# Optimization experiments

Hardware: AMD Instinct MI355X
Metric: run time of the kernel (lower is better)

Reference implementation:

```python
import jax, jax.numpy as jnp
import numpy as np

EMBED_DIM = 1024
NUM_HEADS = 16
HEAD_DIM = EMBED_DIM // NUM_HEADS


def setup_inputs() -> dict:
    key = jax.random.key(0)
    ks = jax.random.split(key, 9)
    B, S, D = 4, 2048, EMBED_DIM
    scale = 1.0 / np.sqrt(D)
    inp = {
        "x": jax.random.normal(ks[0], (B, S, D), dtype=jnp.float32),
        "wq": jax.random.normal(ks[1], (D, D), dtype=jnp.float32) * scale,
        "bq": jnp.zeros((D,), dtype=jnp.float32),
        "wk": jax.random.normal(ks[2], (D, D), dtype=jnp.float32) * scale,
        "bk": jnp.zeros((D,), dtype=jnp.float32),
        "wv": jax.random.normal(ks[3], (D, D), dtype=jnp.float32) * scale,
        "bv": jnp.zeros((D,), dtype=jnp.float32),
        "wo": jax.random.normal(ks[4], (D, D), dtype=jnp.float32) * scale,
        "bo": jnp.zeros((D,), dtype=jnp.float32),
    }
    return inp


def reference(x, wq, bq, wk, bk, wv, bv, wo, bo):
    B, S, D = x.shape
    H, Hd = NUM_HEADS, HEAD_DIM

    def split_heads(t):
        # [B, S, D] -> [B, H, S, Hd]
        return t.reshape(B, S, H, Hd).transpose(0, 2, 1, 3)

    q = split_heads(x @ wq.T + bq)
    k = split_heads(x @ wk.T + bk)
    v = split_heads(x @ wv.T + bv)

    scores = jnp.einsum("bhqd,bhkd->bhqk", q, k) / jnp.sqrt(jnp.float32(Hd))
    attn = jax.nn.softmax(scores, axis=-1)
    out = jnp.einsum("bhqk,bhkd->bhqd", attn, v)  # [B, H, S, Hd]
    out = out.transpose(0, 2, 1, 3).reshape(B, S, D)
    return out @ wo.T + bo
```

## Files before the change

kernel.cpp:

```cpp
#include <hip/hip_runtime.h>
#include <hip/hip_bf16.h>
#include <hip/hip_fp16.h>

typedef _Float16 f16;
typedef f16 f16x8 __attribute__((ext_vector_type(8)));
typedef f16 f16x4 __attribute__((ext_vector_type(4)));
typedef f16 f16x2 __attribute__((ext_vector_type(2)));
typedef float f32x4 __attribute__((ext_vector_type(4)));
typedef float f32x16 __attribute__((ext_vector_type(16)));
typedef unsigned int u32x4 __attribute__((ext_vector_type(4)));
typedef unsigned int u32x2 __attribute__((ext_vector_type(2)));

#define MFMA16(a, b, c) __builtin_amdgcn_mfma_f32_16x16x32_f16(a, b, c, 0, 0, 0)
#define MFMA32(a, b, c) __builtin_amdgcn_mfma_f32_32x32x16_f16(a, b, c, 0, 0, 0)

constexpr int BB = 4, SS = 2048, DD = 1024, HH = 16, HDIM = 64;
constexpr int MM = BB * SS;
constexpr float QSCALE = 0.125f * 1.44269504088896340736f;


__device__ __forceinline__ void gl_lds16(const void* g, void* l) {
  __builtin_amdgcn_global_load_lds((const __attribute__((address_space(1))) void*)g,
                                   (__attribute__((address_space(3))) void*)l, 16, 0, 0);
}

__global__ __launch_bounds__(256) void cvt_all_kernel(const float* __restrict__ x,
                                                      const float* __restrict__ w0,
                                                      const float* __restrict__ w1,
                                                      const float* __restrict__ w2,
                                                      const float* __restrict__ w3,
                                                      f16* xh, f16* o0, f16* o1,
                                                      f16* o2, f16* o3) {
  int bid = blockIdx.x;
  const float* in; f16* out; int idx;
  if (bid < MM * DD / 4 / 256) {
    in = x; out = xh; idx = bid * 256 + threadIdx.x;
  } else {
    int wb = bid - MM * DD / 4 / 256;
    int which = wb >> 10;
    in = which == 0 ? w0 : which == 1 ? w1 : which == 2 ? w2 : w3;
    out = which == 0 ? o0 : which == 1 ? o1 : which == 2 ? o2 : o3;
    idx = (wb & 1023) * 256 + threadIdx.x;
  }
  f32x4 v = reinterpret_cast<const f32x4*>(in)[idx];
  f16x4 o;
  o[0] = (f16)v[0]; o[1] = (f16)v[1]; o[2] = (f16)v[2]; o[3] = (f16)v[3];
  reinterpret_cast<f16x4*>(out)[idx] = o;
}

__device__ __forceinline__ int swz(int row, int slot) {
  return row * 64 + ((slot ^ (row & 7)) << 3);
}

__global__ __launch_bounds__(256) void qkv_kernel(const f16* __restrict__ A,
                                                  const f16* __restrict__ Wq,
                                                  const f16* __restrict__ Wk,
                                                  const f16* __restrict__ Wv,
                                                  const float* __restrict__ bq,
                                                  const float* __restrict__ bk,
                                                  const float* __restrict__ bv,
                                                  f16* __restrict__ Qo,
                                                  f16* __restrict__ Ko,
                                                  f16* __restrict__ Vo) {
  constexpr int K = 1024;
  constexpr int TS = 152;
  __shared__ __align__(16) char smem_raw[128 * TS * 2];
  f16* As = (f16*)smem_raw;
  f16* Ws = As + 128 * 64;

  const int p = blockIdx.x;
  const int bx = (p >> 3) % 24;
  const int by = (p & 7) + 8 * ((p >> 3) / 24);

  const int mat = bx >> 3;
  const f16* W = mat == 0 ? Wq : (mat == 1 ? Wk : Wv);
  const float* bias = mat == 0 ? bq : (mat == 1 ? bk : bv);
  const float scale = mat == 0 ? QSCALE : 1.0f;

  const int tid = threadIdx.x;
  const int m0 = by * 128, n0 = (bx & 7) * 128;
  const int w = tid >> 6, lane = tid & 63;
  const int wm = (w >> 1) * 64, wn = (w & 1) * 64;
  const int g = lane >> 4, r = lane & 15;
  const int srow = lane >> 3;
  const int sslot = (lane & 7) ^ srow;

  f32x4 acc[4][4] = {};

  for (int k0 = 0; k0 < K; k0 += 64) {
#pragma unroll
    for (int i = 0; i < 4; ++i) {
      int rbase = w * 32 + i * 8;
      gl_lds16(A + (size_t)(m0 + rbase + srow) * K + k0 + sslot * 8, As + rbase * 64);
      gl_lds16(W + (size_t)(n0 + rbase + srow) * K + k0 + sslot * 8, Ws + rbase * 64);
    }
    __syncthreads();

#pragma unroll
    for (int ks = 0; ks < 2; ++ks) {
      f16x8 af[4], bf[4];
#pragma unroll
      for (int i = 0; i < 4; ++i) {
        af[i] = *reinterpret_cast<const f16x8*>(As + swz(wm + i * 16 + r, (ks << 2) | g));
        bf[i] = *reinterpret_cast<const f16x8*>(Ws + swz(wn + i * 16 + r, (ks << 2) | g));
      }
#pragma unroll
      for (int i = 0; i < 4; ++i)
#pragma unroll
        for (int j = 0; j < 4; ++j)
          acc[i][j] = MFMA16(af[i], bf[j], acc[i][j]);
    }
    __syncthreads();
  }

  if (mat == 0) {
#pragma unroll
    for (int i = 0; i < 4; ++i)
#pragma unroll
      for (int j = 0; j < 4; ++j)
#pragma unroll
        for (int q = 0; q < 4; ++q) {
          int gm = m0 + wm + i * 16 + g * 4 + q;
          int gn = n0 + wn + j * 16 + r;
          float v = (acc[i][j][q] + bias[gn]) * scale;
          int b = gm >> 11, s = gm & 2047;
          int h = gn >> 6, hd = gn & 63;
          Qo[(((size_t)(b * HH + h)) * SS + s) * HDIM + hd] = (f16)v;
        }
  } else if (mat == 1) {
    __syncthreads();
    f16* T = (f16*)smem_raw;
#pragma unroll
    for (int i = 0; i < 4; ++i)
#pragma unroll
      for (int j = 0; j < 4; ++j)
#pragma unroll
        for (int q = 0; q < 4; ++q) {
          int ml = wm + i * 16 + g * 4 + q;
          int nl = wn + j * 16 + r;
          T[ml * TS + nl] = (f16)(acc[i][j][q] + bias[n0 + nl]);
        }
    __syncthreads();
    const int b = m0 >> 11, sbase = m0 & 2047;
#pragma unroll
    for (int it = 0; it < 8; ++it) {
      int cid = it * 256 + tid;
      int row_s = cid & 127, ns = cid >> 7;
      u32x4 v = *reinterpret_cast<const u32x4*>(T + row_s * TS + ns * 8);
      int gn0 = n0 + ns * 8;
      int h = gn0 >> 6, slot = (gn0 & 63) >> 3;
      int tile = (sbase >> 6) + (row_s >> 6), row = row_s & 63;
      size_t off = ((((size_t)(b * HH + h) * 32 + tile) * 8 + slot) * 64 + row) * 8;
      *reinterpret_cast<u32x4*>(Ko + off) = v;
    }
  } else {
    __syncthreads();
    f16* T = (f16*)smem_raw;
#pragma unroll
    for (int i = 0; i < 4; ++i)
#pragma unroll
      for (int j = 0; j < 4; ++j)
#pragma unroll
        for (int q = 0; q < 4; ++q) {
          int ml = wm + i * 16 + g * 4 + q;
          int nl = wn + j * 16 + r;
          T[nl * TS + ml] = (f16)(acc[i][j][q] + bias[n0 + nl]);
        }
    __syncthreads();
    const int b = m0 >> 11, sbase = m0 & 2047;
#pragma unroll
    for (int it = 0; it < 8; ++it) {
      int cid = it * 256 + tid;
      int hd_l = cid & 127, sl = (cid >> 7) & 7, tl = cid >> 10;
      u32x4 v = *reinterpret_cast<const u32x4*>(T + hd_l * TS + tl * 64 + sl * 8);
      int gn = n0 + hd_l, h = gn >> 6, hd = gn & 63;
      int tile = (sbase >> 6) + tl;
      size_t off = ((((size_t)(b * HH + h) * 32 + tile) * 8 + sl) * 64 + hd) * 8;
      *reinterpret_cast<u32x4*>(Vo + off) = v;
    }
  }
}

__global__ __launch_bounds__(256) void oproj_kernel(const f16* __restrict__ A,
                                                    const f16* __restrict__ W,
                                                    const float* __restrict__ bias,
                                                    float* __restrict__ Out) {
  constexpr int K = 1024, N = 1024;
  __shared__ __align__(16) f16 As[128 * 64];
  __shared__ __align__(16) f16 Ws[128 * 64];

  const int p = blockIdx.x;
  const int bx = (p >> 3) & 7;
  const int by = (p & 7) | ((p >> 6) << 3);

  const int tid = threadIdx.x;
  const int m0 = by * 128, n0 = bx * 128;
  const int w = tid >> 6, lane = tid & 63;
  const int wm = (w >> 1) * 64, wn = (w & 1) * 64;
  const int g = lane >> 4, r = lane & 15;
  const int srow = lane >> 3;
  const int sslot = (lane & 7) ^ srow;

  f32x4 acc[4][4] = {};

  for (int k0 = 0; k0 < K; k0 += 64) {
#pragma unroll
    for (int i = 0; i < 4; ++i) {
      int rbase = w * 32 + i * 8;
      gl_lds16(A + (size_t)(m0 + rbase + srow) * K + k0 + sslot * 8, As + rbase * 64);
      gl_lds16(W + (size_t)(n0 + rbase + srow) * K + k0 + sslot * 8, Ws + rbase * 64);
    }
    __syncthreads();

#pragma unroll
    for (int ks = 0; ks < 2; ++ks) {
      f16x8 af[4], bf[4];
#pragma unroll
      for (int i = 0; i < 4; ++i) {
        af[i] = *reinterpret_cast<const f16x8*>(As + swz(wm + i * 16 + r, (ks << 2) | g));
        bf[i] = *reinterpret_cast<const f16x8*>(Ws + swz(wn + i * 16 + r, (ks << 2) | g));
      }
#pragma unroll
      for (int i = 0; i < 4; ++i)
#pragma unroll
        for (int j = 0; j < 4; ++j)
          acc[i][j] = MFMA16(af[i], bf[j], acc[i][j]);
    }
    __syncthreads();
  }

#pragma unroll
  for (int i = 0; i < 4; ++i)
#pragma unroll
    for (int j = 0; j < 4; ++j)
#pragma unroll
      for (int q = 0; q < 4; ++q) {
        int gm = m0 + wm + i * 16 + g * 4 + q;
        int gn = n0 + wn + j * 16 + r;
        Out[(size_t)gm * N + gn] = acc[i][j][q] + bias[gn];
      }
}

__global__ __launch_bounds__(256, 2) void attn_kernel(const f16* __restrict__ Q,
                                                      const f16* __restrict__ K,
                                                      const f16* __restrict__ Vt,
                                                      f16* __restrict__ AO) {
  __shared__ __align__(16) f16 Kls[2][8 * 512];
  __shared__ __align__(16) f16 Vls[3][8 * 512];
  __shared__ __align__(16) float Lw[4][64];

  const int p = blockIdx.x;
  const int qx = (p >> 3) & 7;
  const int bh = (p & 7) | ((p >> 6) << 3);
  const int q0 = qx * 256;

  const int tid = threadIdx.x;
  const int w = tid >> 6, lane = tid & 63;
  const int q31 = lane & 31;
  const int h = lane >> 5;
  const f16* Kg = K + (size_t)bh * (SS * HDIM);
  const f16* Vg = Vt + (size_t)bh * (SS * HDIM);
  const int s0 = 2 * w;
  const int rofs = h * 512 + q31 * 8;

  const f16* Qg = Q + ((size_t)bh * SS + q0 + w * 64 + q31) * HDIM + 8 * h;
  f16x8 qf[2][4];
#pragma unroll
  for (int f = 0; f < 2; ++f)
#pragma unroll
    for (int m = 0; m < 4; ++m)
      qf[f][m] = *reinterpret_cast<const f16x8*>(Qg + f * 32 * HDIM + 16 * m);

  f32x16 oacc[2][2] = {};
  float lsum0 = 0.f, lsum1 = 0.f;
  unsigned pkP0[8], pkP1[8];

#pragma unroll
  for (int i = 0; i < 2; ++i) {
    int s_idx = s0 + i;
    gl_lds16(Kg + (size_t)(s_idx * 64 + lane) * 8, &Kls[0][s_idx * 512]);
    gl_lds16(Vg + (size_t)(s_idx * 64 + lane) * 8, &Vls[0][s_idx * 512]);
  }
  __syncthreads();

#define QK_PHASE(KC, KB, SC0, SC1)                                                   \
  do {                                                                               \
    _Pragma("unroll") for (int m = 0; m < 4; ++m) {                                  \
      f16x8 kf = *reinterpret_cast<const f16x8*>((KC) + m * 1024 + (KB)*256 + rofs); \
      SC0 = MFMA32(kf, qf[0][m], SC0);                                               \
      SC1 = MFMA32(kf, qf[1][m], SC1);                                               \
    }                                                                                \
  } while (0)

#define PV_PHASE(VPTR, JB)                                                               \
  do {                                                                                   \
    _Pragma("unroll") for (int jl = 0; jl < 2; ++jl) {                                   \
      auto a0 = __builtin_amdgcn_permlane32_swap(pkP0[4 * jl + 0], pkP0[4 * jl + 2],     \
                                                 false, false);                          \
      auto a1 = __builtin_amdgcn_permlane32_swap(pkP0[4 * jl + 1], pkP0[4 * jl + 3],     \
                                                 false, false);                          \
      u32x4 fa = {(unsigned)a0[0], (unsigned)a1[0], (unsigned)a0[1], (unsigned)a1[1]};   \
      f16x8 pa0 = __builtin_bit_cast(f16x8, fa);                                         \
      auto b0 = __builtin_amdgcn_permlane32_swap(pkP1[4 * jl + 0], pkP1[4 * jl + 2],     \
                                                 false, false);                          \
      auto b1 = __builtin_amdgcn_permlane32_swap(pkP1[4 * jl + 1], pkP1[4 * jl + 3],     \
                                                 false, false);                          \
      u32x4 fb = {(unsigned)b0[0], (unsigned)b1[0], (unsigned)b0[1], (unsigned)b1[1]};   \
      f16x8 pa1 = __builtin_bit_cast(f16x8, fb);                                         \
      const int j = (JB) + jl;                                                           \
      _Pragma("unroll") for (int vb = 0; vb < 2; ++vb) {                                 \
        f16x8 vbf = *reinterpret_cast<const f16x8*>((VPTR) + j * 1024 + vb * 256 + rofs);\
        oacc[0][vb] = MFMA32(pa0, vbf, oacc[0][vb]);                                     \
        oacc[1][vb] = MFMA32(pa1, vbf, oacc[1][vb]);                                     \
      }                                                                                  \
    }                                                                                    \
  } while (0)

#define SM_PHASE(SC0, SC1)                                                               \
  do {                                                                                   \
    _Pragma("unroll") for (int rp = 0; rp < 4; ++rp)                                     \
        _Pragma("unroll") for (int pp = 0; pp < 2; ++pp) {                               \
      float a0 = __builtin_amdgcn_exp2f((SC0)[4 * rp + 2 * pp]);                         \
      float a1 = __builtin_amdgcn_exp2f((SC0)[4 * rp + 2 * pp + 1]);                     \
      pkP0[2 * rp + pp] = __builtin_bit_cast(unsigned, __builtin_amdgcn_cvt_pkrtz(a0, a1));\
      float b0 = __builtin_amdgcn_exp2f((SC1)[4 * rp + 2 * pp]);                         \
      float b1 = __builtin_amdgcn_exp2f((SC1)[4 * rp + 2 * pp + 1]);                     \
      pkP1[2 * rp + pp] = __builtin_bit_cast(unsigned, __builtin_amdgcn_cvt_pkrtz(b0, b1));\
    }                                                                                    \
    {                                                                                    \
      f16x2 u01 = __builtin_bit_cast(f16x2, pkP0[0]) + __builtin_bit_cast(f16x2, pkP0[1]);\
      f16x2 u23 = __builtin_bit_cast(f16x2, pkP0[2]) + __builtin_bit_cast(f16x2, pkP0[3]);\
      f16x2 u45 = __builtin_bit_cast(f16x2, pkP0[4]) + __builtin_bit_cast(f16x2, pkP0[5]);\
      f16x2 u67 = __builtin_bit_cast(f16x2, pkP0[6]) + __builtin_bit_cast(f16x2, pkP0[7]);\
      f16x2 ut = (u01 + u23) + (u45 + u67);                                              \
      lsum0 += (float)ut[0] + (float)ut[1];                                              \
    }                                                                                    \
    {                                                                                    \
      f16x2 u01 = __builtin_bit_cast(f16x2, pkP1[0]) + __builtin_bit_cast(f16x2, pkP1[1]);\
      f16x2 u23 = __builtin_bit_cast(f16x2, pkP1[2]) + __builtin_bit_cast(f16x2, pkP1[3]);\
      f16x2 u45 = __builtin_bit_cast(f16x2, pkP1[4]) + __builtin_bit_cast(f16x2, pkP1[5]);\
      f16x2 u67 = __builtin_bit_cast(f16x2, pkP1[6]) + __builtin_bit_cast(f16x2, pkP1[7]);\
      f16x2 ut = (u01 + u23) + (u45 + u67);                                              \
      lsum1 += (float)ut[0] + (float)ut[1];                                              \
    }                                                                                    \
  } while (0)

  for (int t = 0; t < SS / 64; ++t) {
    if (t < SS / 64 - 1) {
      f16* kdst = &Kls[(t + 1) & 1][0];
      f16* vdst = &Vls[(t + 1) % 3][0];
#pragma unroll
      for (int i = 0; i < 2; ++i) {
        int s_idx = s0 + i;
        gl_lds16(Kg + (size_t)((t + 1) * 512 + s_idx * 64 + lane) * 8, kdst + s_idx * 512);
        gl_lds16(Vg + (size_t)((t + 1) * 512 + s_idx * 64 + lane) * 8, vdst + s_idx * 512);
      }
    }
    const f16* Kc = &Kls[t & 1][0];
    const f16* Vcur = &Vls[t % 3][0];
    const f16* Vprev = &Vls[(t + 2) % 3][0];

    {
      f32x16 sc0 = {}, sc1 = {};
      __builtin_amdgcn_s_setprio(1);
      QK_PHASE(Kc, 0, sc0, sc1);
      if (t > 0) PV_PHASE(Vprev, 2);
      __builtin_amdgcn_s_setprio(0);
      SM_PHASE(sc0, sc1);
    }
    {
      f32x16 sc0 = {}, sc1 = {};
      __builtin_amdgcn_s_setprio(1);
      QK_PHASE(Kc, 1, sc0, sc1);
      PV_PHASE(Vcur, 0);
      __builtin_amdgcn_s_setprio(0);
      SM_PHASE(sc0, sc1);
    }
    __syncthreads();
  }

  {
    const f16* Vlast = &Vls[(SS / 64 - 1) % 3][0];
    __builtin_amdgcn_s_setprio(1);
    PV_PHASE(Vlast, 2);
    __builtin_amdgcn_s_setprio(0);
  }

  lsum0 += __shfl_xor(lsum0, 32, 64);
  lsum1 += __shfl_xor(lsum1, 32, 64);
  if (h == 0) {
    Lw[w][q31] = 1.0f / lsum0;
    Lw[w][32 + q31] = 1.0f / lsum1;
  }

  const int b = bh >> 4, head = bh & 15;
#pragma unroll
  for (int f = 0; f < 2; ++f) {
    f32x4 li[4];
#pragma unroll
    for (int rq = 0; rq < 4; ++rq)
      li[rq] = *reinterpret_cast<const f32x4*>(&Lw[w][32 * f + 8 * rq + 4 * h]);
    f16* aobase = AO + ((size_t)(b * SS + q0 + 64 * w + 32 * f)) * DD + head * 64 + q31;
#pragma unroll
    for (int vb = 0; vb < 2; ++vb)
#pragma unroll
      for (int reg = 0; reg < 16; ++reg) {
        int q = (reg & 3) + 8 * (reg >> 2) + 4 * h;
        aobase[(size_t)q * DD + 32 * vb] = (f16)(oacc[f][vb][reg] * li[reg >> 2][reg & 3]);
      }
  }
#undef QK_PHASE
#undef PV_PHASE
#undef SM_PHASE
}

extern "C" void kernel_launch(void* const* d_in, const int* in_sizes, int n_in,
                              void* d_out, int out_size, void* d_ws, size_t ws_size,
                              hipStream_t stream) {
  (void)in_sizes; (void)n_in; (void)out_size; (void)ws_size;
  const float* x  = (const float*)d_in[0];
  const float* wq = (const float*)d_in[1];
  const float* bq = (const float*)d_in[2];
  const float* wk = (const float*)d_in[3];
  const float* bk = (const float*)d_in[4];
  const float* wv = (const float*)d_in[5];
  const float* bv = (const float*)d_in[6];
  const float* wo = (const float*)d_in[7];
  const float* bo = (const float*)d_in[8];
  float* out = (float*)d_out;

  char* ws = (char*)d_ws;
  f16* xh  = (f16*)ws; ws += (size_t)MM * DD * 2;
  f16* wqh = (f16*)ws; ws += (size_t)DD * DD * 2;
  f16* wkh = (f16*)ws; ws += (size_t)DD * DD * 2;
  f16* wvh = (f16*)ws; ws += (size_t)DD * DD * 2;
  f16* woh = (f16*)ws; ws += (size_t)DD * DD * 2;
  f16* Qb  = (f16*)ws; ws += (size_t)MM * DD * 2;
  f16* Kb  = (f16*)ws; ws += (size_t)MM * DD * 2;
  f16* Vtb = (f16*)ws; ws += (size_t)MM * DD * 2;
  f16* AOb = (f16*)ws; ws += (size_t)MM * DD * 2;

  cvt_all_kernel<<<MM * DD / 4 / 256 + 4 * (DD * DD / 4 / 256), 256, 0, stream>>>(
      x, wq, wk, wv, wo, xh, wqh, wkh, wvh, woh);

  qkv_kernel<<<1536, 256, 0, stream>>>(xh, wqh, wkh, wvh, bq, bk, bv, Qb, Kb, Vtb);

  attn_kernel<<<512, 256, 0, stream>>>(Qb, Kb, Vtb, AOb);

  oproj_kernel<<<512, 256, 0, stream>>>(AOb, woh, bo, out);
}
```

Before: 179.7 us.

## Load K/V tiles directly from global memory into registers instead of LDS staging

The attention kernel drops the LDS double/triple buffers for K and V along with the per-iteration __syncthreads. Each wave now loads its own K and V fragments straight from global memory into registers and prefetches the next tile during the softmax phase. This removes the LDS round trip and the block-wide barriers. In exchange, each of the four waves in a block reloads the same K/V data from global memory (relying on cache), and register pressure rises, which may hurt occupancy.

```diff
diff --git a/kernel.cpp b/kernel.cpp
--- a/kernel.cpp
+++ b/kernel.cpp
@@ -245,9 +245,7 @@
                                                       const f16* __restrict__ K,
                                                       const f16* __restrict__ Vt,
                                                       f16* __restrict__ AO) {
-  __shared__ __align__(16) f16 Kls[2][8 * 512];
-  __shared__ __align__(16) f16 Vls[3][8 * 512];
-  __shared__ __align__(16) float Lw[4][64];
+  __shared__ float Lw[4][64];
 
   const int p = blockIdx.x;
   const int qx = (p >> 3) & 7;
@@ -258,10 +256,9 @@
   const int w = tid >> 6, lane = tid & 63;
   const int q31 = lane & 31;
   const int h = lane >> 5;
-  const f16* Kg = K + (size_t)bh * (SS * HDIM);
-  const f16* Vg = Vt + (size_t)bh * (SS * HDIM);
-  const int s0 = 2 * w;
-  const int rofs = h * 512 + q31 * 8;
+
+  const f16* Kl = K + (size_t)bh * (SS * HDIM) + h * 512 + q31 * 8;
+  const f16* Vl = Vt + (size_t)bh * (SS * HDIM) + h * 512 + q31 * 8;
 
   const f16* Qg = Q + ((size_t)bh * SS + q0 + w * 64 + q31) * HDIM + 8 * h;
   f16x8 qf[2][4];
@@ -275,24 +272,21 @@
   float lsum0 = 0.f, lsum1 = 0.f;
   unsigned pkP0[8], pkP1[8];
 
-#pragma unroll
-  for (int i = 0; i < 2; ++i) {
-    int s_idx = s0 + i;
-    gl_lds16(Kg + (size_t)(s_idx * 64 + lane) * 8, &Kls[0][s_idx * 512]);
-    gl_lds16(Vg + (size_t)(s_idx * 64 + lane) * 8, &Vls[0][s_idx * 512]);
-  }
-  __syncthreads();
-
-#define QK_PHASE(KC, KB, SC0, SC1)                                                   \
-  do {                                                                               \
-    _Pragma("unroll") for (int m = 0; m < 4; ++m) {                                  \
-      f16x8 kf = *reinterpret_cast<const f16x8*>((KC) + m * 1024 + (KB)*256 + rofs); \
-      SC0 = MFMA32(kf, qf[0][m], SC0);                                               \
-      SC1 = MFMA32(kf, qf[1][m], SC1);                                               \
-    }                                                                                \
-  } while (0)
-
-#define PV_PHASE(VPTR, JB)                                                               \
+  u32x4 kA[4], kB[4], vLo[4], vHi[4];
+
+#define LD16(PTR) (*reinterpret_cast<const u32x4*>(PTR))
+
+#pragma unroll
+  for (int m = 0; m < 4; ++m) kA[m] = LD16(Kl + m * 1024);
+#pragma unroll
+  for (int m = 0; m < 4; ++m) kB[m] = LD16(Kl + m * 1024 + 256);
+#pragma unroll
+  for (int jl = 0; jl < 2; ++jl)
+#pragma unroll
+    for (int vb = 0; vb < 2; ++vb)
+      vLo[2 * jl + vb] = LD16(Vl + jl * 1024 + vb * 256);
+
+#define PV_CLUSTER(VREG)                                                                 \
   do {                                                                                   \
     _Pragma("unroll") for (int jl = 0; jl < 2; ++jl) {                                   \
       auto a0 = __builtin_amdgcn_permlane32_swap(pkP0[4 * jl + 0], pkP0[4 * jl + 2],     \
@@ -307,16 +301,15 @@
                                                  false, false);                          \
       u32x4 fb = {(unsigned)b0[0], (unsigned)b1[0], (unsigned)b0[1], (unsigned)b1[1]};   \
       f16x8 pa1 = __builtin_bit_cast(f16x8, fb);                                         \
-      const int j = (JB) + jl;                                                           \
       _Pragma("unroll") for (int vb = 0; vb < 2; ++vb) {                                 \
-        f16x8 vbf = *reinterpret_cast<const f16x8*>((VPTR) + j * 1024 + vb * 256 + rofs);\
+        f16x8 vbf = __builtin_bit_cast(f16x8, (VREG)[2 * jl + vb]);                      \
         oacc[0][vb] = MFMA32(pa0, vbf, oacc[0][vb]);                                     \
         oacc[1][vb] = MFMA32(pa1, vbf, oacc[1][vb]);                                     \
       }                                                                                  \
     }                                                                                    \
   } while (0)
 
-#define SM_PHASE(SC0, SC1)                                                               \
+#define SM_CLUSTER(SC0, SC1)                                                             \
   do {                                                                                   \
     _Pragma("unroll") for (int rp = 0; rp < 4; ++rp)                                     \
         _Pragma("unroll") for (int pp = 0; pp < 2; ++pp) {                               \
@@ -346,45 +339,59 @@
   } while (0)
 
   for (int t = 0; t < SS / 64; ++t) {
-    if (t < SS / 64 - 1) {
-      f16* kdst = &Kls[(t + 1) & 1][0];
-      f16* vdst = &Vls[(t + 1) % 3][0];
-#pragma unroll
-      for (int i = 0; i < 2; ++i) {
-        int s_idx = s0 + i;
-        gl_lds16(Kg + (size_t)((t + 1) * 512 + s_idx * 64 + lane) * 8, kdst + s_idx * 512);
-        gl_lds16(Vg + (size_t)((t + 1) * 512 + s_idx * 64 + lane) * 8, vdst + s_idx * 512);
-      }
-    }
-    const f16* Kc = &Kls[t & 1][0];
-    const f16* Vcur = &Vls[t % 3][0];
-    const f16* Vprev = &Vls[(t + 2) % 3][0];
+    const size_t tb = (size_t)t * 4096;
+    const size_t tn = tb + 4096;
 
     {
       f32x16 sc0 = {}, sc1 = {};
       __builtin_amdgcn_s_setprio(1);
-      QK_PHASE(Kc, 0, sc0, sc1);
-      if (t > 0) PV_PHASE(Vprev, 2);
+#pragma unroll
+      for (int m = 0; m < 4; ++m) {
+        f16x8 kf = __builtin_bit_cast(f16x8, kA[m]);
+        sc0 = MFMA32(kf, qf[0][m], sc0);
+        sc1 = MFMA32(kf, qf[1][m], sc1);
+      }
+      if (t > 0) PV_CLUSTER(vHi);
       __builtin_amdgcn_s_setprio(0);
-      SM_PHASE(sc0, sc1);
-    }
+#pragma unroll
+      for (int jl = 0; jl < 2; ++jl)
+#pragma unroll
+        for (int vb = 0; vb < 2; ++vb)
+          vHi[2 * jl + vb] = LD16(Vl + tb + (2 + jl) * 1024 + vb * 256);
+      if (t < SS / 64 - 1) {
+#pragma unroll
+        for (int m = 0; m < 4; ++m) kA[m] = LD16(Kl + tn + m * 1024);
+      }
+      SM_CLUSTER(sc0, sc1);
+    }
+
     {
       f32x16 sc0 = {}, sc1 = {};
       __builtin_amdgcn_s_setprio(1);
-      QK_PHASE(Kc, 1, sc0, sc1);
-      PV_PHASE(Vcur, 0);
+#pragma unroll
+      for (int m = 0; m < 4; ++m) {
+        f16x8 kf = __builtin_bit_cast(f16x8, kB[m]);
+        sc0 = MFMA32(kf, qf[0][m], sc0);
+        sc1 = MFMA32(kf, qf[1][m], sc1);
+      }
+      PV_CLUSTER(vLo);
       __builtin_amdgcn_s_setprio(0);
-      SM_PHASE(sc0, sc1);
-    }
-    __syncthreads();
-  }
-
-  {
-    const f16* Vlast = &Vls[(SS / 64 - 1) % 3][0];
-    __builtin_amdgcn_s_setprio(1);
-    PV_PHASE(Vlast, 2);
-    __builtin_amdgcn_s_setprio(0);
-  }
+      if (t < SS / 64 - 1) {
+#pragma unroll
+        for (int m = 0; m < 4; ++m) kB[m] = LD16(Kl + tn + m * 1024 + 256);
+#pragma unroll
+        for (int jl = 0; jl < 2; ++jl)
+#pragma unroll
+          for (int vb = 0; vb < 2; ++vb)
+            vLo[2 * jl + vb] = LD16(Vl + tn + jl * 1024 + vb * 256);
+      }
+      SM_CLUSTER(sc0, sc1);
+    }
+  }
+
+  __builtin_amdgcn_s_setprio(1);
+  PV_CLUSTER(vHi);
+  __builtin_amdgcn_s_setprio(0);
 
   lsum0 += __shfl_xor(lsum0, 32, 64);
   lsum1 += __shfl_xor(lsum1, 32, 64);
@@ -409,9 +416,9 @@
         aobase[(size_t)q * DD + 32 * vb] = (f16)(oacc[f][vb][reg] * li[reg >> 2][reg & 3]);
       }
   }
-#undef QK_PHASE
-#undef PV_PHASE
-#undef SM_PHASE
+#undef PV_CLUSTER
+#undef SM_CLUSTER
+#undef LD16
 }
 
 extern "C" void kernel_launch(void* const* d_in, const int* in_sizes, int n_in,
```

Result: slower. 184.6 us (+2.7%).

## Replace QKV and output GEMMs with triple-buffered 256x128 eight-wave kernel

Applied to the files above, without the earlier changes.

Merges the QKV and output-projection GEMMs into one templated kernel with 256x128 tiles, 512 threads, and a three-stage LDS ring. Prefetches for tile t+2 are issued between MFMA phases, with vmcnt-based waits and raised wave priority so loads overlap compute. The goal is to hide global-to-LDS latency and raise MFMA density over the single-buffered, sync-heavy originals. In exchange it uses much more LDS per block (about 144 KB), which limits occupancy, and launches fewer blocks (768 and 256), which may underfill the GPU's CUs.

```diff
diff --git a/kernel.cpp b/kernel.cpp
--- a/kernel.cpp
+++ b/kernel.cpp
@@ -48,197 +48,218 @@
   reinterpret_cast<f16x4*>(out)[idx] = o;
 }
 
-__device__ __forceinline__ int swz(int row, int slot) {
-  return row * 64 + ((slot ^ (row & 7)) << 3);
-}
-
-__global__ __launch_bounds__(256) void qkv_kernel(const f16* __restrict__ A,
-                                                  const f16* __restrict__ Wq,
-                                                  const f16* __restrict__ Wk,
-                                                  const f16* __restrict__ Wv,
-                                                  const float* __restrict__ bq,
-                                                  const float* __restrict__ bk,
-                                                  const float* __restrict__ bv,
-                                                  f16* __restrict__ Qo,
-                                                  f16* __restrict__ Ko,
-                                                  f16* __restrict__ Vo) {
-  constexpr int K = 1024;
-  constexpr int TS = 152;
-  __shared__ __align__(16) char smem_raw[128 * TS * 2];
-  f16* As = (f16*)smem_raw;
-  f16* Ws = As + 128 * 64;
+template <bool QKV>
+__global__ __launch_bounds__(512) void gemm8_kernel(const f16* __restrict__ A,
+                                                    const f16* __restrict__ W0,
+                                                    const f16* __restrict__ W1,
+                                                    const f16* __restrict__ W2,
+                                                    const float* __restrict__ b0,
+                                                    const float* __restrict__ b1,
+                                                    const float* __restrict__ b2,
+                                                    void* __restrict__ O0,
+                                                    void* __restrict__ O1,
+                                                    void* __restrict__ O2) {
+  constexpr int NT = 16;
+  constexpr int BUF = 256 * 64 + 128 * 64;
+  __shared__ __align__(16) f16 smem[3 * BUF];
 
   const int p = blockIdx.x;
-  const int bx = (p >> 3) % 24;
-  const int by = (p & 7) + 8 * ((p >> 3) / 24);
-
-  const int mat = bx >> 3;
-  const f16* W = mat == 0 ? Wq : (mat == 1 ? Wk : Wv);
-  const float* bias = mat == 0 ? bq : (mat == 1 ? bk : bv);
-  const float scale = mat == 0 ? QSCALE : 1.0f;
+  const int bl = p >> 3;
+  const int NS = QKV ? 24 : 8;
+  const int nn = bl % NS;
+  const int my = (p & 7) + 8 * (bl / NS);
+  const int mat = QKV ? (nn >> 3) : 0;
+  const int m0 = my * 256;
+  const int n0 = (nn & 7) * 128;
+
+  const f16* W = mat == 0 ? W0 : (mat == 1 ? W1 : W2);
+  const float* bias = mat == 0 ? b0 : (mat == 1 ? b1 : b2);
 
   const int tid = threadIdx.x;
-  const int m0 = by * 128, n0 = (bx & 7) * 128;
   const int w = tid >> 6, lane = tid & 63;
-  const int wm = (w >> 1) * 64, wn = (w & 1) * 64;
+  const int wm = w >> 2, wn = w & 3;
   const int g = lane >> 4, r = lane & 15;
-  const int srow = lane >> 3;
-  const int sslot = (lane & 7) ^ srow;
-
-  f32x4 acc[4][4] = {};
-
-  for (int k0 = 0; k0 < K; k0 += 64) {
-#pragma unroll
-    for (int i = 0; i < 4; ++i) {
-      int rbase = w * 32 + i * 8;
-      gl_lds16(A + (size_t)(m0 + rbase + srow) * K + k0 + sslot * 8, As + rbase * 64);
-      gl_lds16(W + (size_t)(n0 + rbase + srow) * K + k0 + sslot * 8, Ws + rbase * 64);
-    }
+
+  const int srow_a = ((w * 64 + lane) >> 3);
+  const int sc = lane & 7;
+
+  f32x4 acc[8][2] = {};
+
+#define STAGE_A(I, PB, KT)                                                              \
+  do {                                                                                  \
+    int cid_ = ((I)*8 + w) * 64 + lane;                                                 \
+    int row_ = cid_ >> 3, c_ = cid_ & 7;                                                \
+    gl_lds16(A + (size_t)(m0 + row_) * 1024 + (KT) + ((c_ ^ (row_ & 7)) << 3),          \
+             smem + (PB) + ((I)*8 + w) * 512);                                          \
+  } while (0)
+#define STAGE_B(I, PB, KT)                                                              \
+  do {                                                                                  \
+    int cid_ = ((I)*8 + w) * 64 + lane;                                                 \
+    int row_ = cid_ >> 3, c_ = cid_ & 7;                                                \
+    gl_lds16(W + (size_t)(n0 + row_) * 1024 + (KT) + ((c_ ^ (row_ & 7)) << 3),          \
+             smem + (PB) + 256 * 64 + ((I)*8 + w) * 512);                               \
+  } while (0)
+
+#pragma unroll
+  for (int i = 0; i < 4; ++i) STAGE_A(i, 0, 0);
+#pragma unroll
+  for (int i = 0; i < 2; ++i) STAGE_B(i, 0, 0);
+#pragma unroll
+  for (int i = 0; i < 4; ++i) STAGE_A(i, BUF, 64);
+#pragma unroll
+  for (int i = 0; i < 2; ++i) STAGE_B(i, BUF, 64);
+  __builtin_amdgcn_sched_barrier(0);
+  asm volatile("s_waitcnt vmcnt(6)" ::: "memory");
+  __builtin_amdgcn_s_barrier();
+  __builtin_amdgcn_sched_barrier(0);
+
+  for (int t = 0; t < NT; ++t) {
+    const f16* Ab = smem + (t % 3) * BUF;
+    const f16* Wb = Ab + 256 * 64;
+    const int pb = ((t + 2) % 3) * BUF;
+    const int kpf = (t + 2) * 64;
+    const bool do_pf = (t + 2) < NT;
+
+    f16x8 wf[2][2];
+#pragma unroll
+    for (int ks = 0; ks < 2; ++ks)
+#pragma unroll
+      for (int j = 0; j < 2; ++j) {
+        int rowW = wn * 32 + j * 16 + r;
+        wf[ks][j] = *reinterpret_cast<const f16x8*>(
+            Wb + rowW * 64 + (((ks << 2) | g) ^ (rowW & 7)) * 8);
+      }
+
+    if (do_pf) { STAGE_A(0, pb, kpf); STAGE_A(1, pb, kpf); STAGE_B(0, pb, kpf); }
+    __builtin_amdgcn_s_setprio(1);
+#pragma unroll
+    for (int ks = 0; ks < 2; ++ks)
+#pragma unroll
+      for (int i = 0; i < 4; ++i) {
+        int rowA = wm * 128 + i * 16 + r;
+        f16x8 af = *reinterpret_cast<const f16x8*>(
+            Ab + rowA * 64 + (((ks << 2) | g) ^ (rowA & 7)) * 8);
+        acc[i][0] = MFMA16(af, wf[ks][0], acc[i][0]);
+        acc[i][1] = MFMA16(af, wf[ks][1], acc[i][1]);
+      }
+    __builtin_amdgcn_s_setprio(0);
+
+    if (do_pf) { STAGE_A(2, pb, kpf); STAGE_A(3, pb, kpf); STAGE_B(1, pb, kpf); }
+    __builtin_amdgcn_s_setprio(1);
+#pragma unroll
+    for (int ks = 0; ks < 2; ++ks)
+#pragma unroll
+      for (int i = 0; i < 4; ++i) {
+        int rowA = wm * 128 + 64 + i * 16 + r;
+        f16x8 af = *reinterpret_cast<const f16x8*>(
+            Ab + rowA * 64 + (((ks << 2) | g) ^ (rowA & 7)) * 8);
+        acc[4 + i][0] = MFMA16(af, wf[ks][0], acc[4 + i][0]);
+        acc[4 + i][1] = MFMA16(af, wf[ks][1], acc[4 + i][1]);
+      }
+    __builtin_amdgcn_s_setprio(0);
+
+    __builtin_amdgcn_sched_barrier(0);
+    if (t < NT - 2) {
+      asm volatile("s_waitcnt vmcnt(6)" ::: "memory");
+      __builtin_amdgcn_s_barrier();
+    } else if (t == NT - 2) {
+      asm volatile("s_waitcnt vmcnt(0)" ::: "memory");
+      __builtin_amdgcn_s_barrier();
+    }
+    __builtin_amdgcn_sched_barrier(0);
+  }
+#undef STAGE_A
+#undef STAGE_B
+
+  const int sbase = m0 & 2047, bb = m0 >> 11;
+  if constexpr (!QKV) {
+    float* Out = reinterpret_cast<float*>(O0);
+#pragma unroll
+    for (int ii = 0; ii < 8; ++ii) {
+      int rowoff = (ii >> 2) * 64 + (ii & 3) * 16;
+#pragma unroll
+      for (int j = 0; j < 2; ++j)
+#pragma unroll
+        for (int q = 0; q < 4; ++q) {
+          int gm = m0 + wm * 128 + rowoff + g * 4 + q;
+          int gn = n0 + wn * 32 + j * 16 + r;
+          Out[(size_t)gm * 1024 + gn] = acc[ii][j][q] + bias[gn];
+        }
+    }
+  } else if (mat == 0) {
+    f16* Qo = reinterpret_cast<f16*>(O0);
+#pragma unroll
+    for (int ii = 0; ii < 8; ++ii) {
+      int rowoff = (ii >> 2) * 64 + (ii & 3) * 16;
+#pragma unroll
+      for (int j = 0; j < 2; ++j)
+#pragma unroll
+        for (int q = 0; q < 4; ++q) {
+          int gm = m0 + wm * 128 + rowoff + g * 4 + q;
+          int gn = n0 + wn * 32 + j * 16 + r;
+          float v = (acc[ii][j][q] + bias[gn]) * QSCALE;
+          int b = gm >> 11, s = gm & 2047;
+          int hh = gn >> 6, hd = gn & 63;
+          Qo[(((size_t)(b * HH + hh)) * SS + s) * HDIM + hd] = (f16)v;
+        }
+    }
+  } else if (mat == 1) {
+    f16* Ko = reinterpret_cast<f16*>(O1);
     __syncthreads();
-
-#pragma unroll
-    for (int ks = 0; ks < 2; ++ks) {
-      f16x8 af[4], bf[4];
-#pragma unroll
-      for (int i = 0; i < 4; ++i) {
-        af[i] = *reinterpret_cast<const f16x8*>(As + swz(wm + i * 16 + r, (ks << 2) | g));
-        bf[i] = *reinterpret_cast<const f16x8*>(Ws + swz(wn + i * 16 + r, (ks << 2) | g));
-      }
-#pragma unroll
-      for (int i = 0; i < 4; ++i)
-#pragma unroll
-        for (int j = 0; j < 4; ++j)
-          acc[i][j] = MFMA16(af[i], bf[j], acc[i][j]);
+    f16* T = smem;
+#pragma unroll
+    for (int ii = 0; ii < 8; ++ii) {
+      int rowoff = (ii >> 2) * 64 + (ii & 3) * 16;
+#pragma unroll
+      for (int j = 0; j < 2; ++j)
+#pragma unroll
+        for (int q = 0; q < 4; ++q) {
+          int ml = wm * 128 + rowoff + g * 4 + q;
+          int nl = wn * 32 + j * 16 + r;
+          T[ml * 136 + nl] = (f16)(acc[ii][j][q] + bias[n0 + nl]);
+        }
     }
     __syncthreads();
-  }
-
-  if (mat == 0) {
-#pragma unroll
-    for (int i = 0; i < 4; ++i)
-#pragma unroll
-      for (int j = 0; j < 4; ++j)
+#pragma unroll
+    for (int it = 0; it < 8; ++it) {
+      int cid = it * 512 + tid;
+      int row_s = cid & 255, ns = cid >> 8;
+      u32x4 v = *reinterpret_cast<const u32x4*>(T + row_s * 136 + ns * 8);
+      int gn0 = n0 + ns * 8;
+      int hh = gn0 >> 6, slot = (gn0 & 63) >> 3;
+      int tile = (sbase >> 6) + (row_s >> 6), row = row_s & 63;
+      size_t off = ((((size_t)(bb * HH + hh) * 32 + tile) * 8 + slot) * 64 + row) * 8;
+      *reinterpret_cast<u32x4*>(Ko + off) = v;
+    }
+  } else {
+    f16* Vo = reinterpret_cast<f16*>(O2);
+    __syncthreads();
+    f16* T = smem;
+#pragma unroll
+    for (int ii = 0; ii < 8; ++ii) {
+      int rowoff = (ii >> 2) * 64 + (ii & 3) * 16;
+#pragma unroll
+      for (int j = 0; j < 2; ++j)
 #pragma unroll
         for (int q = 0; q < 4; ++q) {
-          int gm = m0 + wm + i * 16 + g * 4 + q;
-          int gn = n0 + wn + j * 16 + r;
-          float v = (acc[i][j][q] + bias[gn]) * scale;
-          int b = gm >> 11, s = gm & 2047;
-          int h = gn >> 6, hd = gn & 63;
-          Qo[(((size_t)(b * HH + h)) * SS + s) * HDIM + hd] = (f16)v;
+          int ml = wm * 128 + rowoff + g * 4 + q;
+          int nl = wn * 32 + j * 16 + r;
+          T[nl * 264 + ml] = (f16)(acc[ii][j][q] + bias[n0 + nl]);
         }
-  } else if (mat == 1) {
+    }
     __syncthreads();
-    f16* T = (f16*)smem_raw;
-#pragma unroll
-    for (int i = 0; i < 4; ++i)
-#pragma unroll
-      for (int j = 0; j < 4; ++j)
-#pragma unroll
-        for (int q = 0; q < 4; ++q) {
-          int ml = wm + i * 16 + g * 4 + q;
-          int nl = wn + j * 16 + r;
-          T[ml * TS + nl] = (f16)(acc[i][j][q] + bias[n0 + nl]);
-        }
-    __syncthreads();
-    const int b = m0 >> 11, sbase = m0 & 2047;
 #pragma unroll
     for (int it = 0; it < 8; ++it) {
-      int cid = it * 256 + tid;
-      int row_s = cid & 127, ns = cid >> 7;
-      u32x4 v = *reinterpret_cast<const u32x4*>(T + row_s * TS + ns * 8);
-      int gn0 = n0 + ns * 8;
-      int h = gn0 >> 6, slot = (gn0 & 63) >> 3;
-      int tile = (sbase >> 6) + (row_s >> 6), row = row_s & 63;
-      size_t off = ((((size_t)(b * HH + h) * 32 + tile) * 8 + slot) * 64 + row) * 8;
-      *reinterpret_cast<u32x4*>(Ko + off) = v;
-    }
-  } else {
-    __syncthreads();
-    f16* T = (f16*)smem_raw;
-#pragma unroll
-    for (int i = 0; i < 4; ++i)
-#pragma unroll
-      for (int j = 0; j < 4; ++j)
-#pragma unroll
-        for (int q = 0; q < 4; ++q) {
-          int ml = wm + i * 16 + g * 4 + q;
-          int nl = wn + j * 16 + r;
-          T[nl * TS + ml] = (f16)(acc[i][j][q] + bias[n0 + nl]);
-        }
-    __syncthreads();
-    const int b = m0 >> 11, sbase = m0 & 2047;
-#pragma unroll
-    for (int it = 0; it < 8; ++it) {
-      int cid = it * 256 + tid;
-      int hd_l = cid & 127, sl = (cid >> 7) & 7, tl = cid >> 10;
-      u32x4 v = *reinterpret_cast<const u32x4*>(T + hd_l * TS + tl * 64 + sl * 8);
-      int gn = n0 + hd_l, h = gn >> 6, hd = gn & 63;
+      int cid = it * 512 + tid;
+      int hd_l = cid & 127, rest = cid >> 7;
+      int sl = rest & 7, tl = rest >> 3;
+      u32x4 v = *reinterpret_cast<const u32x4*>(T + hd_l * 264 + tl * 64 + sl * 8);
+      int gn = n0 + hd_l, hh = gn >> 6, hd = gn & 63;
       int tile = (sbase >> 6) + tl;
-      size_t off = ((((size_t)(b * HH + h) * 32 + tile) * 8 + sl) * 64 + hd) * 8;
+      size_t off = ((((size_t)(bb * HH + hh) * 32 + tile) * 8 + sl) * 64 + hd) * 8;
       *reinterpret_cast<u32x4*>(Vo + off) = v;
     }
   }
-}
-
-__global__ __launch_bounds__(256) void oproj_kernel(const f16* __restrict__ A,
-                                                    const f16* __restrict__ W,
-                                                    const float* __restrict__ bias,
-                                                    float* __restrict__ Out) {
-  constexpr int K = 1024, N = 1024;
-  __shared__ __align__(16) f16 As[128 * 64];
-  __shared__ __align__(16) f16 Ws[128 * 64];
-
-  const int p = blockIdx.x;
-  const int bx = (p >> 3) & 7;
-  const int by = (p & 7) | ((p >> 6) << 3);
-
-  const int tid = threadIdx.x;
-  const int m0 = by * 128, n0 = bx * 128;
-  const int w = tid >> 6, lane = tid & 63;
-  const int wm = (w >> 1) * 64, wn = (w & 1) * 64;
-  const int g = lane >> 4, r = lane & 15;
-  const int srow = lane >> 3;
-  const int sslot = (lane & 7) ^ srow;
-
-  f32x4 acc[4][4] = {};
-
-  for (int k0 = 0; k0 < K; k0 += 64) {
-#pragma unroll
-    for (int i = 0; i < 4; ++i) {
-      int rbase = w * 32 + i * 8;
-      gl_lds16(A + (size_t)(m0 + rbase + srow) * K + k0 + sslot * 8, As + rbase * 64);
-      gl_lds16(W + (size_t)(n0 + rbase + srow) * K + k0 + sslot * 8, Ws + rbase * 64);
-    }
-    __syncthreads();
-
-#pragma unroll
-    for (int ks = 0; ks < 2; ++ks) {
-      f16x8 af[4], bf[4];
-#pragma unroll
-      for (int i = 0; i < 4; ++i) {
-        af[i] = *reinterpret_cast<const f16x8*>(As + swz(wm + i * 16 + r, (ks << 2) | g));
-        bf[i] = *reinterpret_cast<const f16x8*>(Ws + swz(wn + i * 16 + r, (ks << 2) | g));
-      }
-#pragma unroll
-      for (int i = 0; i < 4; ++i)
-#pragma unroll
-        for (int j = 0; j < 4; ++j)
-          acc[i][j] = MFMA16(af[i], bf[j], acc[i][j]);
-    }
-    __syncthreads();
-  }
-
-#pragma unroll
-  for (int i = 0; i < 4; ++i)
-#pragma unroll
-    for (int j = 0; j < 4; ++j)
-#pragma unroll
-      for (int q = 0; q < 4; ++q) {
-        int gm = m0 + wm + i * 16 + g * 4 + q;
-        int gn = n0 + wn + j * 16 + r;
-        Out[(size_t)gm * N + gn] = acc[i][j][q] + bias[gn];
-      }
 }
 
 __global__ __launch_bounds__(256, 2) void attn_kernel(const f16* __restrict__ Q,
@@ -443,9 +464,10 @@
   cvt_all_kernel<<<MM * DD / 4 / 256 + 4 * (DD * DD / 4 / 256), 256, 0, stream>>>(
       x, wq, wk, wv, wo, xh, wqh, wkh, wvh, woh);
 
-  qkv_kernel<<<1536, 256, 0, stream>>>(xh, wqh, wkh, wvh, bq, bk, bv, Qb, Kb, Vtb);
+  gemm8_kernel<true><<<768, 512, 0, stream>>>(xh, wqh, wkh, wvh, bq, bk, bv, Qb, Kb, Vtb);
 
   attn_kernel<<<512, 256, 0, stream>>>(Qb, Kb, Vtb, AOb);
 
-  oproj_kernel<<<512, 256, 0, stream>>>(AOb, woh, bo, out);
+  gemm8_kernel<false><<<256, 512, 0, stream>>>(AOb, woh, nullptr, nullptr, bo, nullptr,
+                                               nullptr, out, nullptr, nullptr);
 }
```

Result: no change. 180.0 us (+0.2%).
